# Performance work log

Measured on AMD Instinct MI355X. Metric: run time of the kernel, lower is better.

The kernel has to match this reference:

```python
import jax, jax.numpy as jnp
import numpy as np

N = 3072
D = 256
H = 8
HD = D // H
E = 98304
NUM_EDGE_TYPES = 16
MAX_DIST = 10
MAX_DEG = 512
BIAS_SCALE = 10.0
ATTN_TEMP = 0.5
EPS = 1e-5


def _ln(x, g, b):
    m = x.mean(-1, keepdims=True)
    v = ((x - m) ** 2).mean(-1, keepdims=True)
    return (x - m) / jnp.sqrt(v + EPS) * g + b


def setup_inputs() -> dict:
    key = jax.random.key(0)
    ks = jax.random.split(key, 24)
    f32 = jnp.float32
    x = jax.random.normal(ks[0], (N, D), f32)
    edge_index = jax.random.randint(ks[1], (2, E), 0, N)
    edge_types = jax.random.randint(ks[2], (E,), 0, NUM_EDGE_TYPES)
    pos_encoding = jax.random.uniform(ks[3], (N, N), f32)
    edge_weights = jax.random.uniform(ks[4], (E,), f32)
    s = 0.02
    Wq = jax.random.normal(ks[5], (D, D), f32) * s
    Wk = jax.random.normal(ks[6], (D, D), f32) * s
    Wv = jax.random.normal(ks[7], (D, D), f32) * s
    Wo = jax.random.normal(ks[8], (D, D), f32) * s
    bq = jnp.zeros((D,), f32); bk = jnp.zeros((D,), f32)
    bv = jnp.zeros((D,), f32); bo = jnp.zeros((D,), f32)
    spd_table = jax.random.normal(ks[9], (MAX_DIST + 2, H), f32) * s
    edge_type_table = jax.random.normal(ks[10], (NUM_EDGE_TYPES, H), f32) * s
    self_loop_bias = jnp.ones((H,), f32)
    in_deg_emb = jax.random.normal(ks[11], (MAX_DEG + 1, D), f32) * s
    out_deg_emb = jax.random.normal(ks[12], (MAX_DEG + 1, D), f32) * s
    degree_scale = jnp.ones((1,), f32)
    ln1_g = jnp.ones((D,), f32); ln1_b = jnp.zeros((D,), f32)
    ln2_g = jnp.ones((D,), f32); ln2_b = jnp.zeros((D,), f32)
    W1 = jax.random.normal(ks[13], (D, 4 * D), f32) * s
    b1 = jnp.zeros((4 * D,), f32)
    W2 = jax.random.normal(ks[14], (4 * D, D), f32) * s
    b2 = jnp.zeros((D,), f32)
    return dict(x=x, edge_index=edge_index, edge_types=edge_types,
                pos_encoding=pos_encoding, edge_weights=edge_weights,
                Wq=Wq, bq=bq, Wk=Wk, bk=bk, Wv=Wv, bv=bv, Wo=Wo, bo=bo,
                spd_table=spd_table, edge_type_table=edge_type_table,
                self_loop_bias=self_loop_bias, in_deg_emb=in_deg_emb,
                out_deg_emb=out_deg_emb, degree_scale=degree_scale,
                ln1_g=ln1_g, ln1_b=ln1_b, ln2_g=ln2_g, ln2_b=ln2_b,
                W1=W1, b1=b1, W2=W2, b2=b2)


def reference(x, edge_index, edge_types, pos_encoding, edge_weights,
              Wq, bq, Wk, bk, Wv, bv, Wo, bo,
              spd_table, edge_type_table, self_loop_bias,
              in_deg_emb, out_deg_emb, degree_scale,
              ln1_g, ln1_b, ln2_g, ln2_b, W1, b1, W2, b2):
    src, dst = edge_index[0], edge_index[1]
    ones = jnp.ones((E,), jnp.int32)
    deg_out = jnp.clip(jax.ops.segment_sum(ones, src, num_segments=N), 0, MAX_DEG)
    deg_in = jnp.clip(jax.ops.segment_sum(ones, dst, num_segments=N), 0, MAX_DEG)
    x = x + (in_deg_emb[deg_in] + out_deg_emb[deg_out]) * degree_scale
    xn = _ln(x, ln1_g, ln1_b)
    q = (xn @ Wq + bq).reshape(N, H, HD).transpose(1, 0, 2)  # [H,N,hd]
    k = (xn @ Wk + bk).reshape(N, H, HD).transpose(1, 0, 2)
    v = (xn @ Wv + bv).reshape(N, H, HD).transpose(1, 0, 2)
    # structural attention bias [H,N,N]
    spd = pos_encoding[:, :N]
    bucket = jnp.where(spd == 0, 0,
             jnp.where(spd > 1.0, MAX_DIST + 1,
                       jnp.clip(spd * MAX_DIST, 1, MAX_DIST).astype(jnp.int32)))
    bias = spd_table[bucket].transpose(2, 0, 1) * BIAS_SCALE
    bias = bias + self_loop_bias[:, None, None] * jnp.eye(N, dtype=bias.dtype)
    e_bias = edge_type_table[edge_types] + edge_weights[:, None] * (2.0 * BIAS_SCALE)  # [E,H]
    bias = bias.at[:, src, dst].add((e_bias * BIAS_SCALE).T)
    # SDPA path: q/temp, k/temp then 1/sqrt(hd) scale -> 1/(temp^2*sqrt(hd))
    scale = 1.0 / (ATTN_TEMP * ATTN_TEMP * np.sqrt(HD).astype(np.float32))
    scores = jnp.einsum('hnd,hmd->hnm', q, k) * scale + bias
    attn = jax.nn.softmax(scores, axis=-1)
    attn_out = jnp.einsum('hnm,hmd->hnd', attn, v).transpose(1, 0, 2).reshape(N, D)
    x = x + attn_out @ Wo + bo
    y = _ln(x, ln2_g, ln2_b)
    y = jax.nn.gelu(y @ W1 + b1, approximate=False) @ W2 + b2
    return x + y
```

## Files before the change

### kernel.cpp

```cpp
#include <hip/hip_runtime.h>
#include <hip/hip_bf16.h>

#define NN 3072
#define DM 256
#define NH 8
#define HDIM 32
#define NE 98304
#define DFF 1024
#define MAXDEG 512
#define NIT 192
#define NJT 48
#define JSPLIT 4

typedef short bf16x8 __attribute__((ext_vector_type(8)));
typedef float f32x4 __attribute__((ext_vector_type(4)));
typedef unsigned short u16;
typedef unsigned int u32;

#define MFMA16 __builtin_amdgcn_mfma_f32_16x16x32_bf16

__device__ __forceinline__ u16 f2bf(float f){
  u32 u = __builtin_bit_cast(u32, f);
  u32 r = (u + 0x7FFFu + ((u >> 16) & 1u)) >> 16;
  return (u16)r;
}
__device__ __forceinline__ u32 cvtpk(float lo, float hi){
  u32 r; asm("v_cvt_pk_bf16_f32 %0, %1, %2" : "=v"(r) : "v"(lo), "v"(hi)); return r;
}

__global__ void k_deg(const int* __restrict__ src, const int* __restrict__ dst,
                      int* __restrict__ deg_out, int* __restrict__ deg_in,
                      int* __restrict__ bcnt){
  int e = blockIdx.x * 256 + threadIdx.x;
  if (e < NE){
    int s = src[e], d = dst[e];
    atomicAdd(&deg_out[s], 1);
    atomicAdd(&deg_in[d], 1);
    atomicAdd(&bcnt[(s >> 4) * NJT + (d >> 6)], 1);
  }
}

__global__ __launch_bounds__(1024)
void k_scan(const int* __restrict__ cnt, int* __restrict__ ptr){
  __shared__ int sc[1024];
  int t = threadIdx.x;
  int loc[9]; int s = 0;
  #pragma unroll
  for (int u = 0; u < 9; u++){ loc[u] = cnt[t*9 + u]; s += loc[u]; }
  sc[t] = s;
  __syncthreads();
  for (int off = 1; off < 1024; off <<= 1){
    int v = (t >= off) ? sc[t-off] : 0;
    __syncthreads();
    sc[t] += v;
    __syncthreads();
  }
  int run = sc[t] - s;
  #pragma unroll
  for (int u = 0; u < 9; u++){ ptr[t*9 + u] = run; run += loc[u]; }
  if (t == 1023) ptr[9216] = run;
}

__global__ void k_scatter(const int* __restrict__ src, const int* __restrict__ dst,
                          const int* __restrict__ types, const float* __restrict__ w,
                          const int* __restrict__ bptr, int* __restrict__ bfill,
                          u16* __restrict__ meta, float* __restrict__ ews){
  int e = blockIdx.x * 256 + threadIdx.x;
  if (e < NE){
    int s = src[e], d = dst[e];
    int b = (s >> 4) * NJT + (d >> 6);
    int slot = bptr[b] + atomicAdd(&bfill[b], 1);
    meta[slot] = (u16)((s & 15) | ((d & 63) << 4) | (types[e] << 10));
    ews[slot] = w[e];
  }
}

__global__ __launch_bounds__(1024)
void k_bucket(const float* __restrict__ pos, unsigned char* __restrict__ bktP){
  int j = blockIdx.x * 1024 + threadIdx.x;
  int i = blockIdx.y;
  float spv = pos[(size_t)i*NN + j];
  int bkt;
  if (spv == 0.f) bkt = 0;
  else if (spv > 1.f) bkt = 11;
  else { float cc = fminf(fmaxf(spv * 10.f, 1.f), 10.f); bkt = (int)cc; }
  bktP[(size_t)i*NN + (j & ~63) + (j & 15)*4 + ((j >> 4) & 3)] = (unsigned char)bkt;
}

__global__ __launch_bounds__(256)
void k_trans(const float* __restrict__ Wq, const float* __restrict__ Wk,
             const float* __restrict__ Wv, const float* __restrict__ Wo,
             const float* __restrict__ W1, const float* __restrict__ W2,
             u16* __restrict__ Wqkvot, u16* __restrict__ W1t, u16* __restrict__ W2t){
  __shared__ u16 t_[32][33];
  int bt = blockIdx.x;
  const float* srcm; u16* dstm; int K, N, kt, nt;
  if (bt < 256){
    int m = bt >> 6, r = bt & 63; kt = r >> 3; nt = r & 7; K = 256; N = 256;
    srcm = (m==0)?Wq:(m==1)?Wk:(m==2)?Wv:Wo; dstm = Wqkvot + m*65536;
  } else if (bt < 512){
    int r = bt - 256; kt = r >> 5; nt = r & 31; K = 256; N = 1024; srcm = W1; dstm = W1t;
  } else {
    int r = bt - 512; kt = r >> 3; nt = r & 7; K = 1024; N = 256; srcm = W2; dstm = W2t;
  }
  int tx = threadIdx.x & 31, ty = threadIdx.x >> 5;
  #pragma unroll
  for (int s = 0; s < 4; s++)
    t_[ty + 8*s][tx] = f2bf(srcm[(size_t)(kt*32 + ty + 8*s)*N + nt*32 + tx]);
  __syncthreads();
  #pragma unroll
  for (int s = 0; s < 4; s++)
    dstm[(size_t)(nt*32 + ty + 8*s)*K + kt*32 + tx] = t_[tx][ty + 8*s];
}

__global__ __launch_bounds__(256)
void k_ln(const float* __restrict__ in, const int* __restrict__ deg_in,
          const int* __restrict__ deg_out, const float* __restrict__ in_emb,
          const float* __restrict__ out_emb, const float* __restrict__ dscale,
          const float* __restrict__ g, const float* __restrict__ b,
          float* __restrict__ save_f32, u16* __restrict__ out_bf){
  int i = blockIdx.x, c = threadIdx.x;
  size_t idx = (size_t)i*DM + c;
  float val = in[idx];
  if (deg_in){
    int di = min(deg_in[i], MAXDEG), dg = min(deg_out[i], MAXDEG);
    val += (in_emb[(size_t)di*DM + c] + out_emb[(size_t)dg*DM + c]) * dscale[0];
    save_f32[idx] = val;
  }
  float s = val, s2 = val*val;
  #pragma unroll
  for (int off = 32; off; off >>= 1){
    s  += __shfl_xor(s, off);
    s2 += __shfl_xor(s2, off);
  }
  __shared__ float red[8];
  int lane = c & 63, w = c >> 6;
  if (lane == 0){ red[w] = s; red[4+w] = s2; }
  __syncthreads();
  s  = red[0] + red[1] + red[2] + red[3];
  s2 = red[4] + red[5] + red[6] + red[7];
  float mean = s * (1.f/256.f);
  float var = s2 * (1.f/256.f) - mean*mean;
  float xn = (val - mean) * rsqrtf(var + 1e-5f) * g[c] + b[c];
  out_bf[idx] = f2bf(xn);
}

__global__ __launch_bounds__(256)
void k_gemm(const u16* __restrict__ A, const u16* __restrict__ Bt,
            const float* __restrict__ b0, const float* __restrict__ b1,
            const float* __restrict__ b2, const float* __restrict__ res,
            void* __restrict__ out, void* __restrict__ out2,
            int K, int Ncols, int mode){
  __shared__ u16 sA[64][72];
  __shared__ u16 sB[64][72];
  const int tid = threadIdx.x, lane = tid & 63, wid = tid >> 6;
  const int m0 = blockIdx.y * 64, n0 = blockIdx.x * 64;
  const int wr = (wid >> 1) * 32, wc = (wid & 1) * 32;
  const int srow = tid >> 2, scol = (tid & 3) * 16;
  const int fr = lane & 15, fg = lane >> 4;
  f32x4 acc00 = {0,0,0,0}, acc01 = {0,0,0,0}, acc10 = {0,0,0,0}, acc11 = {0,0,0,0};
  for (int k0 = 0; k0 < K; k0 += 64){
    __syncthreads();
    *(bf16x8*)&sA[srow][scol]     = *(const bf16x8*)&A[(size_t)(m0+srow)*K + k0 + scol];
    *(bf16x8*)&sA[srow][scol + 8] = *(const bf16x8*)&A[(size_t)(m0+srow)*K + k0 + scol + 8];
    *(bf16x8*)&sB[srow][scol]     = *(const bf16x8*)&Bt[(size_t)(n0+srow)*K + k0 + scol];
    *(bf16x8*)&sB[srow][scol + 8] = *(const bf16x8*)&Bt[(size_t)(n0+srow)*K + k0 + scol + 8];
    __syncthreads();
    #pragma unroll
    for (int kk = 0; kk < 2; kk++){
      bf16x8 a0  = *(const bf16x8*)&sA[wr + fr][kk*32 + fg*8];
      bf16x8 a1  = *(const bf16x8*)&sA[wr + 16 + fr][kk*32 + fg*8];
      bf16x8 b0f = *(const bf16x8*)&sB[wc + fr][kk*32 + fg*8];
      bf16x8 b1f = *(const bf16x8*)&sB[wc + 16 + fr][kk*32 + fg*8];
      acc00 = MFMA16(a0, b0f, acc00, 0, 0, 0);
      acc01 = MFMA16(a0, b1f, acc01, 0, 0, 0);
      acc10 = MFMA16(a1, b0f, acc10, 0, 0, 0);
      acc11 = MFMA16(a1, b1f, acc11, 0, 0, 0);
    }
  }
  #pragma unroll
  for (int fm = 0; fm < 2; fm++)
  #pragma unroll
  for (int fn = 0; fn < 2; fn++){
    f32x4 c = (fm==0) ? ((fn==0) ? acc00 : acc01) : ((fn==0) ? acc10 : acc11);
    #pragma unroll
    for (int r = 0; r < 4; r++){
      int row = m0 + wr + fm*16 + fg*4 + r;
      int col = n0 + wc + fn*16 + fr;
      if (mode == 5){
        int seg = col >> 8, cn = col & 255;
        const float* bp = (seg==0) ? b0 : (seg==1) ? b1 : b2;
        float val = c[r] + bp[cn];
        if (seg == 0) val *= 0.70710678f;
        if (seg < 2) ((u16*)out)[(size_t)seg*NN*DM + (size_t)row*DM + cn] = f2bf(val);
        else         ((u16*)out2)[(size_t)cn*NN + row] = f2bf(val);
      } else {
        float val = c[r] + b0[col];
        size_t idx = (size_t)row*Ncols + col;
        if (mode == 2) ((float*)out)[idx] = res[idx] + val;
        else           ((u16*)out)[idx] = f2bf(0.5f*val*(1.f + erff(val*0.70710678f)));
      }
    }
  }
}

__global__ __launch_bounds__(512)
void k_attn(const u16* __restrict__ qb, const u16* __restrict__ kb, const u16* __restrict__ vT,
            const unsigned char* __restrict__ bktP,
            const float* __restrict__ spd_table, const float* __restrict__ slb,
            const u16* __restrict__ meta, const float* __restrict__ ews,
            const float* __restrict__ ett, const int* __restrict__ bptr,
            float* __restrict__ opart, float* __restrict__ mpart, float* __restrict__ lpart){
  __shared__ float s_sc[NH][16][68];
  __shared__ float s_spdw[NH][32];
  __shared__ float s_ettw[NH][32];
  const int tid = threadIdx.x, lane = tid & 63, h = tid >> 6;
  const int it = blockIdx.x, jc = blockIdx.y;
  const int i0 = it * 16;
  if (lane < 12) s_spdw[h][lane] = spd_table[lane*8 + h] * 10.f;
  if (lane < 16) s_ettw[h][lane] = ett[lane*8 + h] * 10.f;
  const float slbh = slb[h];
  const int fr = lane & 15, fg = lane >> 4;
  bf16x8 qv = *(const bf16x8*)&qb[(size_t)(i0 + fr)*DM + h*HDIM + fg*8];
  float (*sc)[68] = s_sc[h];
  f32x4 o0 = {0,0,0,0}, o1 = {0,0,0,0};
  float m_run = -3.0e38f, l_run = 0.f;

  for (int jt = jc*(NJT/JSPLIT); jt < (jc+1)*(NJT/JSPLIT); ++jt){
    const int j0 = jt * 64;
    bf16x8 kf0 = *(const bf16x8*)&kb[(size_t)(j0      + fr)*DM + h*HDIM + fg*8];
    bf16x8 kf1 = *(const bf16x8*)&kb[(size_t)(j0 + 16 + fr)*DM + h*HDIM + fg*8];
    bf16x8 kf2 = *(const bf16x8*)&kb[(size_t)(j0 + 32 + fr)*DM + h*HDIM + fg*8];
    bf16x8 kf3 = *(const bf16x8*)&kb[(size_t)(j0 + 48 + fr)*DM + h*HDIM + fg*8];
    uchar4 bk0 = *(const uchar4*)&bktP[(size_t)(i0 + fg*4 + 0)*NN + j0 + fr*4];
    uchar4 bk1 = *(const uchar4*)&bktP[(size_t)(i0 + fg*4 + 1)*NN + j0 + fr*4];
    uchar4 bk2 = *(const uchar4*)&bktP[(size_t)(i0 + fg*4 + 2)*NN + j0 + fr*4];
    uchar4 bk3 = *(const uchar4*)&bktP[(size_t)(i0 + fg*4 + 3)*NN + j0 + fr*4];
    f32x4 z = {0,0,0,0};
    f32x4 s0 = MFMA16(qv, kf0, z, 0, 0, 0);
    f32x4 s1 = MFMA16(qv, kf1, z, 0, 0, 0);
    f32x4 s2 = MFMA16(qv, kf2, z, 0, 0, 0);
    f32x4 s3 = MFMA16(qv, kf3, z, 0, 0, 0);
    unsigned char bb[4][4] = {{bk0.x,bk0.y,bk0.z,bk0.w},{bk1.x,bk1.y,bk1.z,bk1.w},
                              {bk2.x,bk2.y,bk2.z,bk2.w},{bk3.x,bk3.y,bk3.z,bk3.w}};
    const bool dg_tile = (j0 == (i0 & ~63));
    #pragma unroll
    for (int r = 0; r < 4; r++){
      int row = fg*4 + r;
      #pragma unroll
      for (int c2 = 0; c2 < 4; c2++){
        int col = c2*16 + fr;
        float sv = (c2==0) ? s0[r] : (c2==1) ? s1[r] : (c2==2) ? s2[r] : s3[r];
        float val = sv + s_spdw[h][(int)bb[r][c2]];
        if (dg_tile && (i0 + row == j0 + col)) val += slbh;
        sc[row][col] = val;
      }
    }
    {
      int e0 = bptr[it*NJT + jt], e1 = bptr[it*NJT + jt + 1];
      for (int ix = e0 + lane; ix < e1; ix += 64){
        u16 me = meta[ix];
        int il = me & 15, jl = (me >> 4) & 63, tp = me >> 10;
        atomicAdd(&sc[il][jl], s_ettw[h][tp] + 200.f * ews[ix]);
      }
    }
    float v[16];
    { f32x4 a = *(const f32x4*)&sc[fr][fg*8];
      v[0]=a[0]; v[1]=a[1]; v[2]=a[2]; v[3]=a[3]; }
    { f32x4 a = *(const f32x4*)&sc[fr][fg*8 + 4];
      v[4]=a[0]; v[5]=a[1]; v[6]=a[2]; v[7]=a[3]; }
    { f32x4 a = *(const f32x4*)&sc[fr][32 + fg*8];
      v[8]=a[0]; v[9]=a[1]; v[10]=a[2]; v[11]=a[3]; }
    { f32x4 a = *(const f32x4*)&sc[fr][32 + fg*8 + 4];
      v[12]=a[0]; v[13]=a[1]; v[14]=a[2]; v[15]=a[3]; }
    float mx = v[0];
    #pragma unroll
    for (int t = 1; t < 16; t++) mx = fmaxf(mx, v[t]);
    mx = fmaxf(mx, __shfl_xor(mx, 16));
    mx = fmaxf(mx, __shfl_xor(mx, 32));
    float mnew = fmaxf(m_run, mx);
    float fac = __expf(m_run - mnew);
    float p[16], ps = 0.f;
    #pragma unroll
    for (int t = 0; t < 16; t++){ p[t] = __expf(v[t] - mnew); ps += p[t]; }
    ps += __shfl_xor(ps, 16);
    ps += __shfl_xor(ps, 32);
    l_run = l_run * fac + ps;
    m_run = mnew;
    float f0 = __shfl(fac, fg*4 + 0);
    float f1 = __shfl(fac, fg*4 + 1);
    float f2 = __shfl(fac, fg*4 + 2);
    float f3 = __shfl(fac, fg*4 + 3);
    o0[0]*=f0; o0[1]*=f1; o0[2]*=f2; o0[3]*=f3;
    o1[0]*=f0; o1[1]*=f1; o1[2]*=f2; o1[3]*=f3;
    union { u32 w[4]; bf16x8 v8; } pa0u, pa1u;
    #pragma unroll
    for (int t = 0; t < 4; t++){
      pa0u.w[t] = cvtpk(p[2*t], p[2*t+1]);
      pa1u.w[t] = cvtpk(p[8 + 2*t], p[9 + 2*t]);
    }
    bf16x8 vf00 = *(const bf16x8*)&vT[(size_t)(h*HDIM      + fr)*NN + j0      + fg*8];
    bf16x8 vf01 = *(const bf16x8*)&vT[(size_t)(h*HDIM      + fr)*NN + j0 + 32 + fg*8];
    bf16x8 vf10 = *(const bf16x8*)&vT[(size_t)(h*HDIM + 16 + fr)*NN + j0      + fg*8];
    bf16x8 vf11 = *(const bf16x8*)&vT[(size_t)(h*HDIM + 16 + fr)*NN + j0 + 32 + fg*8];
    o0 = MFMA16(pa0u.v8, vf00, o0, 0, 0, 0);
    o0 = MFMA16(pa1u.v8, vf01, o0, 0, 0, 0);
    o1 = MFMA16(pa0u.v8, vf10, o1, 0, 0, 0);
    o1 = MFMA16(pa1u.v8, vf11, o1, 0, 0, 0);
  }

  float* ob = opart + (size_t)jc*NN*DM;
  #pragma unroll
  for (int r = 0; r < 4; r++){
    size_t row = i0 + fg*4 + r;
    ob[row*DM + h*HDIM + fr]      = o0[r];
    ob[row*DM + h*HDIM + 16 + fr] = o1[r];
  }
  if (fg == 0){
    mpart[jc*NN*NH + (i0 + fr)*NH + h] = m_run;
    lpart[jc*NN*NH + (i0 + fr)*NH + h] = l_run;
  }
}

__global__ __launch_bounds__(256)
void k_reduce(const float* __restrict__ opart, const float* __restrict__ mpart,
              const float* __restrict__ lpart, u16* __restrict__ aob){
  int row = blockIdx.x, col = threadIdx.x, h = col >> 5;
  float m[JSPLIT], l[JSPLIT];
  float M = -3.0e38f;
  #pragma unroll
  for (int jc = 0; jc < JSPLIT; jc++){
    m[jc] = mpart[jc*NN*NH + row*NH + h];
    l[jc] = lpart[jc*NN*NH + row*NH + h];
    M = fmaxf(M, m[jc]);
  }
  float L = 0.f, acc = 0.f;
  #pragma unroll
  for (int jc = 0; jc < JSPLIT; jc++){
    float w = __expf(m[jc] - M);
    L += l[jc] * w;
    acc += opart[(size_t)jc*NN*DM + (size_t)row*DM + col] * w;
  }
  aob[(size_t)row*DM + col] = f2bf(acc / L);
}

extern "C" void kernel_launch(void* const* d_in, const int* in_sizes, int n_in,
                              void* d_out, int out_size, void* d_ws, size_t ws_size,
                              hipStream_t stream){
  const float* x     = (const float*)d_in[0];
  const int*   ei    = (const int*)d_in[1];
  const int*   etyp  = (const int*)d_in[2];
  const float* pos   = (const float*)d_in[3];
  const float* ewin  = (const float*)d_in[4];
  const float* Wq    = (const float*)d_in[5];
  const float* bq    = (const float*)d_in[6];
  const float* Wk    = (const float*)d_in[7];
  const float* bk    = (const float*)d_in[8];
  const float* Wv    = (const float*)d_in[9];
  const float* bv    = (const float*)d_in[10];
  const float* Wo    = (const float*)d_in[11];
  const float* bo    = (const float*)d_in[12];
  const float* spd   = (const float*)d_in[13];
  const float* ett   = (const float*)d_in[14];
  const float* slb   = (const float*)d_in[15];
  const float* inde  = (const float*)d_in[16];
  const float* outde = (const float*)d_in[17];
  const float* dsc   = (const float*)d_in[18];
  const float* ln1g  = (const float*)d_in[19];
  const float* ln1b  = (const float*)d_in[20];
  const float* ln2g  = (const float*)d_in[21];
  const float* ln2b  = (const float*)d_in[22];
  const float* W1    = (const float*)d_in[23];
  const float* b1    = (const float*)d_in[24];
  const float* W2    = (const float*)d_in[25];
  const float* b2    = (const float*)d_in[26];
  const int* src = ei;
  const int* dst = ei + NE;

  char* p = (char*)d_ws;
  auto alloc = [&](size_t bytes) -> void* {
    void* r = (void*)p;
    p += (bytes + 255) & ~(size_t)255;
    return r;
  };
  int*  deg_in  = (int*)alloc(NN*4);
  int*  deg_out = (int*)alloc(NN*4);
  int*  bcnt    = (int*)alloc(9216*4);
  int*  bfill   = (int*)alloc(9216*4);
  int*  bptr    = (int*)alloc(9217*4);
  u16*  meta    = (u16*)alloc(NE*2);
  float* ews    = (float*)alloc(NE*4);
  unsigned char* bktP = (unsigned char*)alloc((size_t)NN*NN);
  float* xb     = (float*)alloc((size_t)NN*DM*4);
  float* x2     = (float*)alloc((size_t)NN*DM*4);
  u16*  xnb     = (u16*)alloc((size_t)NN*DM*2);
  u16*  x2nb    = (u16*)alloc((size_t)NN*DM*2);
  u16*  qb      = (u16*)alloc((size_t)NN*DM*2);
  u16*  kb      = (u16*)alloc((size_t)NN*DM*2);
  u16*  vT      = (u16*)alloc((size_t)NN*DM*2);
  u16*  aob     = (u16*)alloc((size_t)NN*DM*2);
  u16*  h1b     = (u16*)alloc((size_t)NN*DFF*2);
  float* opart  = (float*)alloc((size_t)JSPLIT*NN*DM*4);
  float* mpart  = (float*)alloc((size_t)JSPLIT*NN*NH*4);
  float* lpart  = (float*)alloc((size_t)JSPLIT*NN*NH*4);
  u16*  Wqkvot  = (u16*)alloc(4*65536*2);
  u16*  W1t     = (u16*)alloc(262144*2);
  u16*  W2t     = (u16*)alloc(262144*2);

  hipMemsetAsync(deg_in, 0, (2*NN + 2*9216)*4, stream);

  k_deg<<<NE/256, 256, 0, stream>>>(src, dst, deg_out, deg_in, bcnt);
  k_scan<<<1, 1024, 0, stream>>>(bcnt, bptr);
  k_scatter<<<NE/256, 256, 0, stream>>>(src, dst, etyp, ewin, bptr, bfill, meta, ews);
  k_bucket<<<dim3(3, NN), 1024, 0, stream>>>(pos, bktP);
  k_trans<<<768, 256, 0, stream>>>(Wq, Wk, Wv, Wo, W1, W2, Wqkvot, W1t, W2t);
  k_ln<<<NN, 256, 0, stream>>>(x, deg_in, deg_out, inde, outde, dsc, ln1g, ln1b, xb, xnb);

  k_gemm<<<dim3(12, 48), 256, 0, stream>>>(xnb, Wqkvot, bq, bk, bv, nullptr,
                                           qb, vT, DM, 768, 5);

  k_attn<<<dim3(NIT, JSPLIT), 512, 0, stream>>>(qb, kb, vT, bktP, spd, slb, meta, ews,
                                                ett, bptr, opart, mpart, lpart);
  k_reduce<<<NN, 256, 0, stream>>>(opart, mpart, lpart, aob);

  u16* Wot = Wqkvot + 3*65536;
  k_gemm<<<dim3(4, 48), 256, 0, stream>>>(aob, Wot, bo, nullptr, nullptr, xb,
                                          x2, nullptr, DM, DM, 2);
  k_ln<<<NN, 256, 0, stream>>>(x2, nullptr, nullptr, nullptr, nullptr, nullptr,
                               ln2g, ln2b, nullptr, x2nb);
  k_gemm<<<dim3(16, 48), 256, 0, stream>>>(x2nb, W1t, b1, nullptr, nullptr, nullptr,
                                           h1b, nullptr, DM, DFF, 3);
  k_gemm<<<dim3(4, 48), 256, 0, stream>>>(h1b, W2t, b2, nullptr, nullptr, x2,
                                          d_out, nullptr, DFF, DM, 2);
}
```

Measured before the change: 313.9 us.

## Split attention blocks by head halves and software-prefetch next K/bias tile

The attention kernel now launches 256-thread blocks covering four heads each, with a third grid dimension selecting the head half, and requests higher occupancy through launch bounds. Inside the loop it prefetches the next tile's K fragments and bucket bytes into registers, and issues the V loads and edge-range reads early so their latency overlaps the score MFMAs and softmax. This adds register pressure and duplicates the bucket-byte reads across the two head halves.

Measured after the change: 399.4 us. +27.2%, slower.

```diff
diff --git a/kernel.cpp b/kernel.cpp
--- a/kernel.cpp
+++ b/kernel.cpp
@@ -204,38 +204,63 @@
   }
 }
 
-__global__ __launch_bounds__(512)
+__global__ __launch_bounds__(256, 5)
 void k_attn(const u16* __restrict__ qb, const u16* __restrict__ kb, const u16* __restrict__ vT,
             const unsigned char* __restrict__ bktP,
             const float* __restrict__ spd_table, const float* __restrict__ slb,
             const u16* __restrict__ meta, const float* __restrict__ ews,
             const float* __restrict__ ett, const int* __restrict__ bptr,
             float* __restrict__ opart, float* __restrict__ mpart, float* __restrict__ lpart){
-  __shared__ float s_sc[NH][16][68];
-  __shared__ float s_spdw[NH][32];
-  __shared__ float s_ettw[NH][32];
-  const int tid = threadIdx.x, lane = tid & 63, h = tid >> 6;
+  __shared__ float s_sc[4][16][68];
+  __shared__ float s_spdw[4][32];
+  __shared__ float s_ettw[4][32];
+  const int tid = threadIdx.x, lane = tid & 63, w = tid >> 6;
+  const int h = (blockIdx.z << 2) | w;
   const int it = blockIdx.x, jc = blockIdx.y;
   const int i0 = it * 16;
-  if (lane < 12) s_spdw[h][lane] = spd_table[lane*8 + h] * 10.f;
-  if (lane < 16) s_ettw[h][lane] = ett[lane*8 + h] * 10.f;
+  if (lane < 12) s_spdw[w][lane] = spd_table[lane*8 + h] * 10.f;
+  if (lane < 16) s_ettw[w][lane] = ett[lane*8 + h] * 10.f;
   const float slbh = slb[h];
   const int fr = lane & 15, fg = lane >> 4;
   bf16x8 qv = *(const bf16x8*)&qb[(size_t)(i0 + fr)*DM + h*HDIM + fg*8];
-  float (*sc)[68] = s_sc[h];
+  float (*sc)[68] = s_sc[w];
   f32x4 o0 = {0,0,0,0}, o1 = {0,0,0,0};
   float m_run = -3.0e38f, l_run = 0.f;
 
-  for (int jt = jc*(NJT/JSPLIT); jt < (jc+1)*(NJT/JSPLIT); ++jt){
+  const int jt0 = jc * (NJT/JSPLIT), jt1 = jt0 + NJT/JSPLIT;
+
+  bf16x8 kf0, kf1, kf2, kf3;
+  uchar4 bk0, bk1, bk2, bk3;
+  {
+    const int j0 = jt0 * 64;
+    kf0 = *(const bf16x8*)&kb[(size_t)(j0      + fr)*DM + h*HDIM + fg*8];
+    kf1 = *(const bf16x8*)&kb[(size_t)(j0 + 16 + fr)*DM + h*HDIM + fg*8];
+    kf2 = *(const bf16x8*)&kb[(size_t)(j0 + 32 + fr)*DM + h*HDIM + fg*8];
+    kf3 = *(const bf16x8*)&kb[(size_t)(j0 + 48 + fr)*DM + h*HDIM + fg*8];
+    bk0 = *(const uchar4*)&bktP[(size_t)(i0 + fg*4 + 0)*NN + j0 + fr*4];
+    bk1 = *(const uchar4*)&bktP[(size_t)(i0 + fg*4 + 1)*NN + j0 + fr*4];
+    bk2 = *(const uchar4*)&bktP[(size_t)(i0 + fg*4 + 2)*NN + j0 + fr*4];
+    bk3 = *(const uchar4*)&bktP[(size_t)(i0 + fg*4 + 3)*NN + j0 + fr*4];
+  }
+
+  #pragma unroll 2
+  for (int jt = jt0; jt < jt1; ++jt){
     const int j0 = jt * 64;
-    bf16x8 kf0 = *(const bf16x8*)&kb[(size_t)(j0      + fr)*DM + h*HDIM + fg*8];
-    bf16x8 kf1 = *(const bf16x8*)&kb[(size_t)(j0 + 16 + fr)*DM + h*HDIM + fg*8];
-    bf16x8 kf2 = *(const bf16x8*)&kb[(size_t)(j0 + 32 + fr)*DM + h*HDIM + fg*8];
-    bf16x8 kf3 = *(const bf16x8*)&kb[(size_t)(j0 + 48 + fr)*DM + h*HDIM + fg*8];
-    uchar4 bk0 = *(const uchar4*)&bktP[(size_t)(i0 + fg*4 + 0)*NN + j0 + fr*4];
-    uchar4 bk1 = *(const uchar4*)&bktP[(size_t)(i0 + fg*4 + 1)*NN + j0 + fr*4];
-    uchar4 bk2 = *(const uchar4*)&bktP[(size_t)(i0 + fg*4 + 2)*NN + j0 + fr*4];
-    uchar4 bk3 = *(const uchar4*)&bktP[(size_t)(i0 + fg*4 + 3)*NN + j0 + fr*4];
+    int jn = j0 + 64; if (jn > NN - 64) jn = NN - 64;
+    bf16x8 nkf0 = *(const bf16x8*)&kb[(size_t)(jn      + fr)*DM + h*HDIM + fg*8];
+    bf16x8 nkf1 = *(const bf16x8*)&kb[(size_t)(jn + 16 + fr)*DM + h*HDIM + fg*8];
+    bf16x8 nkf2 = *(const bf16x8*)&kb[(size_t)(jn + 32 + fr)*DM + h*HDIM + fg*8];
+    bf16x8 nkf3 = *(const bf16x8*)&kb[(size_t)(jn + 48 + fr)*DM + h*HDIM + fg*8];
+    uchar4 nbk0 = *(const uchar4*)&bktP[(size_t)(i0 + fg*4 + 0)*NN + jn + fr*4];
+    uchar4 nbk1 = *(const uchar4*)&bktP[(size_t)(i0 + fg*4 + 1)*NN + jn + fr*4];
+    uchar4 nbk2 = *(const uchar4*)&bktP[(size_t)(i0 + fg*4 + 2)*NN + jn + fr*4];
+    uchar4 nbk3 = *(const uchar4*)&bktP[(size_t)(i0 + fg*4 + 3)*NN + jn + fr*4];
+    bf16x8 vf00 = *(const bf16x8*)&vT[(size_t)(h*HDIM      + fr)*NN + j0      + fg*8];
+    bf16x8 vf01 = *(const bf16x8*)&vT[(size_t)(h*HDIM      + fr)*NN + j0 + 32 + fg*8];
+    bf16x8 vf10 = *(const bf16x8*)&vT[(size_t)(h*HDIM + 16 + fr)*NN + j0      + fg*8];
+    bf16x8 vf11 = *(const bf16x8*)&vT[(size_t)(h*HDIM + 16 + fr)*NN + j0 + 32 + fg*8];
+    int e0 = bptr[it*NJT + jt], e1 = bptr[it*NJT + jt + 1];
+
     f32x4 z = {0,0,0,0};
     f32x4 s0 = MFMA16(qv, kf0, z, 0, 0, 0);
     f32x4 s1 = MFMA16(qv, kf1, z, 0, 0, 0);
@@ -251,18 +276,15 @@
       for (int c2 = 0; c2 < 4; c2++){
         int col = c2*16 + fr;
         float sv = (c2==0) ? s0[r] : (c2==1) ? s1[r] : (c2==2) ? s2[r] : s3[r];
-        float val = sv + s_spdw[h][(int)bb[r][c2]];
+        float val = sv + s_spdw[w][(int)bb[r][c2]];
         if (dg_tile && (i0 + row == j0 + col)) val += slbh;
         sc[row][col] = val;
       }
     }
-    {
-      int e0 = bptr[it*NJT + jt], e1 = bptr[it*NJT + jt + 1];
-      for (int ix = e0 + lane; ix < e1; ix += 64){
-        u16 me = meta[ix];
-        int il = me & 15, jl = (me >> 4) & 63, tp = me >> 10;
-        atomicAdd(&sc[il][jl], s_ettw[h][tp] + 200.f * ews[ix]);
-      }
+    for (int ix = e0 + lane; ix < e1; ix += 64){
+      u16 me = meta[ix];
+      int il = me & 15, jl = (me >> 4) & 63, tp = me >> 10;
+      atomicAdd(&sc[il][jl], s_ettw[w][tp] + 200.f * ews[ix]);
     }
     float v[16];
     { f32x4 a = *(const f32x4*)&sc[fr][fg*8];
@@ -293,20 +315,18 @@
     float f3 = __shfl(fac, fg*4 + 3);
     o0[0]*=f0; o0[1]*=f1; o0[2]*=f2; o0[3]*=f3;
     o1[0]*=f0; o1[1]*=f1; o1[2]*=f2; o1[3]*=f3;
-    union { u32 w[4]; bf16x8 v8; } pa0u, pa1u;
+    union { u32 wd[4]; bf16x8 v8; } pa0u, pa1u;
     #pragma unroll
     for (int t = 0; t < 4; t++){
-      pa0u.w[t] = cvtpk(p[2*t], p[2*t+1]);
-      pa1u.w[t] = cvtpk(p[8 + 2*t], p[9 + 2*t]);
+      pa0u.wd[t] = cvtpk(p[2*t], p[2*t+1]);
+      pa1u.wd[t] = cvtpk(p[8 + 2*t], p[9 + 2*t]);
     }
-    bf16x8 vf00 = *(const bf16x8*)&vT[(size_t)(h*HDIM      + fr)*NN + j0      + fg*8];
-    bf16x8 vf01 = *(const bf16x8*)&vT[(size_t)(h*HDIM      + fr)*NN + j0 + 32 + fg*8];
-    bf16x8 vf10 = *(const bf16x8*)&vT[(size_t)(h*HDIM + 16 + fr)*NN + j0      + fg*8];
-    bf16x8 vf11 = *(const bf16x8*)&vT[(size_t)(h*HDIM + 16 + fr)*NN + j0 + 32 + fg*8];
     o0 = MFMA16(pa0u.v8, vf00, o0, 0, 0, 0);
     o0 = MFMA16(pa1u.v8, vf01, o0, 0, 0, 0);
     o1 = MFMA16(pa0u.v8, vf10, o1, 0, 0, 0);
     o1 = MFMA16(pa1u.v8, vf11, o1, 0, 0, 0);
+    kf0 = nkf0; kf1 = nkf1; kf2 = nkf2; kf3 = nkf3;
+    bk0 = nbk0; bk1 = nbk1; bk2 = nbk2; bk3 = nbk3;
   }
 
   float* ob = opart + (size_t)jc*NN*DM;
@@ -419,8 +439,8 @@
   k_gemm<<<dim3(12, 48), 256, 0, stream>>>(xnb, Wqkvot, bq, bk, bv, nullptr,
                                            qb, vT, DM, 768, 5);
 
-  k_attn<<<dim3(NIT, JSPLIT), 512, 0, stream>>>(qb, kb, vT, bktP, spd, slb, meta, ews,
-                                                ett, bptr, opart, mpart, lpart);
+  k_attn<<<dim3(NIT, JSPLIT, 2), 256, 0, stream>>>(qb, kb, vT, bktP, spd, slb, meta, ews,
+                                                   ett, bptr, opart, mpart, lpart);
   k_reduce<<<NN, 256, 0, stream>>>(opart, mpart, lpart, aob);
 
   u16* Wot = Wqkvot + 3*65536;
```
